# Performance work log

Hardware: AMD Instinct MI355X
Metric: run time of the kernel (lower is better)

The kernel has to match this reference:

```python
import jax, jax.numpy as jnp
import numpy as np

LEAK = 0.3          # config['leak_rate']
LAST_N = 8          # config['last_n_outputs']


def setup_inputs() -> dict:
    key = jax.random.key(0)
    k1, k2, k3, k4, k5 = jax.random.split(key, 5)
    B, T, F, H, O = 256, 1000, 64, 1024, 10
    x = jax.random.normal(k1, (B, T, F), dtype=jnp.float32)
    w_in = jax.random.normal(k2, (F, H), dtype=jnp.float32) * 0.2
    # reservoir matrix scaled to spectral radius ~0.9 (randn HxH has radius ~sqrt(H))
    w_r = jax.random.normal(k3, (H, H), dtype=jnp.float32) * (0.9 / np.sqrt(H))
    w_lin = jax.random.normal(k4, (O, H * LAST_N), dtype=jnp.float32) * 0.02
    b_lin = jax.random.normal(k5, (O,), dtype=jnp.float32) * 0.02
    return {"x": x, "w_in": w_in, "w_r": w_r, "w_lin": w_lin, "b_lin": b_lin}


def _esn_forward(x, w_in, w_r, w_lin, b_lin):
    B, T, F = x.shape
    H = w_in.shape[1]
    n = LAST_N
    # t = 0: h_0 = h_hat (no leaky combine per original code)
    h = jnp.tanh(x[:, 0, :] @ w_in)

    def step(h, xt):
        h_hat = jnp.tanh(xt @ w_in + h @ w_r)
        return (1.0 - LEAK) * h + LEAK * h_hat

    # steps 1 .. T-n-1: carry only, no outputs stored
    def body_nohist(h, xt):
        return step(h, xt), None

    xs_mid = jnp.swapaxes(x[:, 1:T - n, :], 0, 1)   # [T-n-1, B, F]
    h, _ = jax.lax.scan(body_nohist, h, xs_mid)

    # steps T-n .. T-1: keep states (out_list in original)
    def body_hist(h, xt):
        h = step(h, xt)
        return h, h

    xs_tail = jnp.swapaxes(x[:, T - n:, :], 0, 1)   # [n, B, F]
    _, hs = jax.lax.scan(body_hist, h, xs_tail)     # [n, B, H]

    # torch.cat(out_list, dim=1): oldest kept state first -> [B, n*H]
    feats = jnp.transpose(hs, (1, 0, 2)).reshape(B, n * H)
    return feats @ w_lin.T + b_lin


def reference(x, w_in, w_r, w_lin, b_lin):
    return _esn_forward(x, w_in, w_r, w_lin, b_lin)
```

## Files before the change

kernel.cpp:

```cpp
#include <hip/hip_runtime.h>
#include <math.h>

#define LEAK   0.3f
#define ONEML  0.7f

typedef unsigned short u16;
typedef unsigned int   u32;
typedef unsigned long long u64;
typedef __attribute__((ext_vector_type(4))) float f32x4;
typedef __attribute__((ext_vector_type(8))) short s16x8;

constexpr int B = 256, T = 1000, F = 64, H = 1024, O = 10, NTAIL = 8;
constexpr int TSTART  = T - NTAIL;
constexpr int KS      = 34;
constexpr int PSTRIDE = 1096;

constexpr size_t OFF_PACKED = 0;
constexpr size_t OFF_HGL    = 0x240000;
constexpr size_t OFF_FLAGS  = 0x340000;
constexpr size_t OFF_FEATS  = 0x344000;

__device__ __forceinline__ u16 f2bf(float f) {
  union { float f; u32 u; } v; v.f = f;
  u32 r = v.u + 0x7fffu + ((v.u >> 16) & 1u);
  return (u16)(r >> 16);
}

__device__ __forceinline__ float ftanh(float s) {
  const float sc = fminf(fmaxf(s, -9.0f), 9.0f);
  const float e2 = __builtin_amdgcn_exp2f(sc * 2.8853900817779268f);
  return 1.0f - 2.0f * __builtin_amdgcn_rcpf(e2 + 1.0f);
}

__global__ void esn_pack(const float* __restrict__ w_in, const float* __restrict__ w_r,
                         u16* __restrict__ packed) {
  int gid = blockIdx.x * 256 + threadIdx.x;
  if (gid >= 64 * KS * 64) return;
  int lane = gid & 63;
  int ks   = (gid >> 6) % KS;
  int nt   = gid / (KS * 64);
  int n    = nt * 16 + (lane & 15);
  int g    = lane >> 4;
  u16 v[8];
  #pragma unroll
  for (int jj = 0; jj < 8; ++jj) {
    int kk = 8 * g + jj;
    float w;
    if (ks < 2) w = w_in[(ks * 32 + kk) * H + n];
    else        w = w_r[((ks - 2) * 32 + kk) * H + n];
    v[jj] = f2bf(w);
  }
  u64* dst = (u64*)(packed + (size_t)gid * 8);
  dst[0] = ((const u64*)v)[0];
  dst[1] = ((const u64*)v)[1];
}

__global__ __launch_bounds__(256, 1) void esn_recur(const float* __restrict__ x,
    const u16* __restrict__ packed, u16* __restrict__ hgl,
    u32* __restrict__ flags, float* __restrict__ feats) {
  __shared__ u16 panel[2][16][PSTRIDE];
  __shared__ u16 forcepad[6144];

  const int tid  = threadIdx.x;
  const int lane = tid & 63, wv = tid >> 6;
  const int ci   = blockIdx.x >> 4;
  const int cj   = blockIdx.x & 15;
  const int g    = lane >> 4, m16 = lane & 15;
  const int nt   = cj * 4 + wv;
  const int cc   = nt * 16 + m16;
  const int bbase = ci * 16;
  const bool ownCols = ((tid >> 4) == cj);

  s16x8 bfrag[KS];
  #pragma unroll
  for (int ks = 0; ks < KS; ++ks)
    bfrag[ks] = *(const s16x8*)(packed + (((size_t)nt * KS + ks) * 64 + lane) * 8);

  float hreg[4] = {0.f, 0.f, 0.f, 0.f};

  for (int t = 0; t < T; ++t) {
    const int buf = t & 1;
    const int nb  = buf ^ 1;

    {
      const int r = tid >> 4;
      const int c = (tid & 15) * 4;
      const float4 v = *(const float4*)(x + (((size_t)(bbase + r)) * T + t) * (size_t)F + c);
      u16 o[4] = { f2bf(v.x), f2bf(v.y), f2bf(v.z), f2bf(v.w) };
      *(u64*)&panel[buf][r][c] = *(const u64*)o;
    }

    if (t > 0) {
      const u32 target = (u32)t;
      u32* fp = &flags[ci * 64 + lane];
      int guard = 0;
      for (;;) {
        u32 fv = __hip_atomic_load(fp, __ATOMIC_RELAXED, __HIP_MEMORY_SCOPE_AGENT);
        if (__all((int)(fv >= target))) break;
        if (++guard > (1 << 16)) break;
      }
      asm volatile("" ::: "memory");
    }

    if (t == 0) {
      #pragma unroll
      for (int it = 0; it < 16; ++it)
        *(u64*)&panel[buf][it][64 + tid * 4] = 0ULL;
    } else if (!ownCols) {
      const int pb = (t + 1) & 1;
      u64 vb[16];
      #pragma unroll
      for (int it = 0; it < 16; ++it)
        vb[it] = __hip_atomic_load(
            (const u64*)(hgl + ((((size_t)pb * 16 + ci) * 16 + it) * H + tid * 4)),
            __ATOMIC_RELAXED, __HIP_MEMORY_SCOPE_AGENT);
      #pragma unroll
      for (int it = 0; it < 16; ++it)
        *(u64*)&panel[buf][it][64 + tid * 4] = vb[it];
    }
    __syncthreads();

    f32x4 acc0 = {0.f,0.f,0.f,0.f}, acc1 = {0.f,0.f,0.f,0.f};
    #pragma unroll
    for (int ks = 0; ks < KS; ++ks) {
      s16x8 a = *(const s16x8*)&panel[buf][m16][ks * 32 + g * 8];
      if (ks & 1) acc1 = __builtin_amdgcn_mfma_f32_16x16x32_bf16(a, bfrag[ks], acc1, 0, 0, 0);
      else        acc0 = __builtin_amdgcn_mfma_f32_16x16x32_bf16(a, bfrag[ks], acc0, 0, 0, 0);
    }

    #pragma unroll
    for (int r = 0; r < 4; ++r) {
      const float s  = acc0[r] + acc1[r];
      const float th = ftanh(s);
      const float hn = (t == 0) ? th : (ONEML * hreg[r] + LEAK * th);
      hreg[r] = hn;
      const int rr = g * 4 + r;
      panel[nb][rr][64 + cc] = f2bf(hn);
      if (t >= TSTART)
        feats[((size_t)(bbase + rr)) * (H * NTAIL) + (t - TSTART) * H + cc] = hn;
    }

    asm volatile("s_waitcnt lgkmcnt(0)" ::: "memory");
    {
      const int r  = lane >> 2;
      const int c4 = (lane & 3) * 4;
      const u64 v = *(const u64*)&panel[nb][r][64 + nt * 16 + c4];
      __hip_atomic_store(
          (u64*)(hgl + ((((size_t)buf * 16 + ci) * 16 + r) * H + nt * 16 + c4)),
          v, __ATOMIC_RELAXED, __HIP_MEMORY_SCOPE_AGENT);
    }

    asm volatile("s_waitcnt vmcnt(0)" ::: "memory");
    if (lane == 0)
      __hip_atomic_store(&flags[ci * 64 + nt], (u32)(t + 1),
                         __ATOMIC_RELAXED, __HIP_MEMORY_SCOPE_AGENT);
  }
  if (tid == 255) ((volatile u16*)forcepad)[0] = (u16)lane;
}

__global__ __launch_bounds__(256) void esn_out(const float* __restrict__ feats,
    const float* __restrict__ w_lin, const float* __restrict__ b_lin,
    float* __restrict__ out) {
  const int b = blockIdx.x;
  const int tid = threadIdx.x;
  const int lane = tid & 63, wv = tid >> 6;
  float p[O];
  #pragma unroll
  for (int o = 0; o < O; ++o) p[o] = 0.f;
  const float* fr = feats + (size_t)b * (H * NTAIL);
  for (int idx = tid; idx < H * NTAIL; idx += 256) {
    const float f = fr[idx];
    #pragma unroll
    for (int o = 0; o < O; ++o) p[o] += f * w_lin[o * (H * NTAIL) + idx];
  }
  __shared__ float red[O][4];
  #pragma unroll
  for (int o = 0; o < O; ++o) {
    float v = p[o];
    for (int off = 32; off > 0; off >>= 1) v += __shfl_down(v, off);
    if (lane == 0) red[o][wv] = v;
  }
  __syncthreads();
  if (tid < O)
    out[b * O + tid] = red[tid][0] + red[tid][1] + red[tid][2] + red[tid][3] + b_lin[tid];
}

extern "C" void kernel_launch(void* const* d_in, const int* in_sizes, int n_in,
                              void* d_out, int out_size, void* d_ws, size_t ws_size,
                              hipStream_t stream) {
  const float* x     = (const float*)d_in[0];
  const float* w_in  = (const float*)d_in[1];
  const float* w_r   = (const float*)d_in[2];
  const float* w_lin = (const float*)d_in[3];
  const float* b_lin = (const float*)d_in[4];
  char* ws = (char*)d_ws;
  u16* packed = (u16*)(ws + OFF_PACKED);
  u16* hgl    = (u16*)(ws + OFF_HGL);
  u32* flags  = (u32*)(ws + OFF_FLAGS);
  float* feats= (float*)(ws + OFF_FEATS);
  float* out  = (float*)d_out;

  hipMemsetAsync(flags, 0, 4096 * sizeof(u32), stream);
  esn_pack<<<(64 * KS * 64 + 255) / 256, 256, 0, stream>>>(w_in, w_r, packed);

  void* args[] = { (void*)&x, (void*)&packed, (void*)&hgl, (void*)&flags, (void*)&feats };
  hipError_t rc = hipLaunchCooperativeKernel((void*)esn_recur, dim3(256), dim3(256),
                                             args, 0, stream);
  if (rc != hipSuccess)
    esn_recur<<<dim3(256), dim3(256), 0, stream>>>(x, packed, hgl, flags, feats);

  esn_out<<<B, 256, 0, stream>>>(feats, w_lin, b_lin, out);
}
```

Before: 3.270 ms.

## Replace store-drain before flag with per-column checksum validation of exchanged hidden state

Removes the vmcnt(0) wait that made each wave's hidden-state stores land before it published its step flag. Each column-tile now also writes a 17th row holding a per-column bf16 checksum XORed with the step number. Readers reload the 16 rows until the checksum matches, so a flag that becomes visible before its data is tolerated. Flags shrink to u16. This trades one full memory-fence stall per step for extra checksum arithmetic, an additional row load, and possible retry loops. Checksum collisions could silently let stale data through.

```diff
diff --git a/kernel.cpp b/kernel.cpp
--- a/kernel.cpp
+++ b/kernel.cpp
@@ -14,11 +14,13 @@
 constexpr int TSTART  = T - NTAIL;
 constexpr int KS      = 34;
 constexpr int PSTRIDE = 1096;
+constexpr int HROWS   = 17;
+
 
 constexpr size_t OFF_PACKED = 0;
 constexpr size_t OFF_HGL    = 0x240000;
-constexpr size_t OFF_FLAGS  = 0x340000;
-constexpr size_t OFF_FEATS  = 0x344000;
+constexpr size_t OFF_FLAGS  = 0x350000;
+constexpr size_t OFF_FEATS  = 0x354000;
 
 __device__ __forceinline__ u16 f2bf(float f) {
   union { float f; u32 u; } v; v.f = f;
@@ -57,7 +59,7 @@
 
 __global__ __launch_bounds__(256, 1) void esn_recur(const float* __restrict__ x,
     const u16* __restrict__ packed, u16* __restrict__ hgl,
-    u32* __restrict__ flags, float* __restrict__ feats) {
+    u16* __restrict__ flags, float* __restrict__ feats) {
   __shared__ u16 panel[2][16][PSTRIDE];
   __shared__ u16 forcepad[6144];
 
@@ -91,11 +93,11 @@
     }
 
     if (t > 0) {
-      const u32 target = (u32)t;
-      u32* fp = &flags[ci * 64 + lane];
+      const u16 target = (u16)t;
+      const u16* fp = flags + ci * 64 + lane;
       int guard = 0;
       for (;;) {
-        u32 fv = __hip_atomic_load(fp, __ATOMIC_RELAXED, __HIP_MEMORY_SCOPE_AGENT);
+        u16 fv = __hip_atomic_load(fp, __ATOMIC_RELAXED, __HIP_MEMORY_SCOPE_AGENT);
         if (__all((int)(fv >= target))) break;
         if (++guard > (1 << 16)) break;
       }
@@ -107,13 +109,37 @@
       for (int it = 0; it < 16; ++it)
         *(u64*)&panel[buf][it][64 + tid * 4] = 0ULL;
     } else if (!ownCols) {
+      const u32 stp = (u32)t & 0xffffu;
       const int pb = (t + 1) & 1;
-      u64 vb[16];
+      const u16* rbase = hgl + (((size_t)pb * 16 + ci) * HROWS) * H + tid * 4;
+      u64 vb[16], ck;
       #pragma unroll
       for (int it = 0; it < 16; ++it)
-        vb[it] = __hip_atomic_load(
-            (const u64*)(hgl + ((((size_t)pb * 16 + ci) * 16 + it) * H + tid * 4)),
-            __ATOMIC_RELAXED, __HIP_MEMORY_SCOPE_AGENT);
+        vb[it] = __hip_atomic_load((const u64*)(rbase + (size_t)it * H),
+                                   __ATOMIC_RELAXED, __HIP_MEMORY_SCOPE_AGENT);
+      ck = __hip_atomic_load((const u64*)(rbase + (size_t)16 * H),
+                             __ATOMIC_RELAXED, __HIP_MEMORY_SCOPE_AGENT);
+      int guard = 0;
+      for (;;) {
+        u32 bad = 0;
+        #pragma unroll
+        for (int c = 0; c < 4; ++c) {
+          u32 s = 0;
+          #pragma unroll
+          for (int it = 0; it < 16; ++it)
+            s += (u32)((vb[it] >> (16 * c)) & 0xffffu);
+          const u32 expect = (s & 0xffffu) ^ stp;
+          if (((u32)(ck >> (16 * c)) & 0xffffu) != expect) bad = 1;
+        }
+        if (!bad) break;
+        if (++guard > 4096) break;
+        #pragma unroll
+        for (int it = 0; it < 16; ++it)
+          vb[it] = __hip_atomic_load((const u64*)(rbase + (size_t)it * H),
+                                     __ATOMIC_RELAXED, __HIP_MEMORY_SCOPE_AGENT);
+        ck = __hip_atomic_load((const u64*)(rbase + (size_t)16 * H),
+                               __ATOMIC_RELAXED, __HIP_MEMORY_SCOPE_AGENT);
+      }
       #pragma unroll
       for (int it = 0; it < 16; ++it)
         *(u64*)&panel[buf][it][64 + tid * 4] = vb[it];
@@ -128,31 +154,39 @@
       else        acc0 = __builtin_amdgcn_mfma_f32_16x16x32_bf16(a, bfrag[ks], acc0, 0, 0, 0);
     }
 
+    u32 cs = 0;
     #pragma unroll
     for (int r = 0; r < 4; ++r) {
       const float s  = acc0[r] + acc1[r];
       const float th = ftanh(s);
       const float hn = (t == 0) ? th : (ONEML * hreg[r] + LEAK * th);
       hreg[r] = hn;
+      const u16 hb = f2bf(hn);
+      cs += (u32)hb;
       const int rr = g * 4 + r;
-      panel[nb][rr][64 + cc] = f2bf(hn);
+      panel[nb][rr][64 + cc] = hb;
       if (t >= TSTART)
         feats[((size_t)(bbase + rr)) * (H * NTAIL) + (t - TSTART) * H + cc] = hn;
     }
+    cs += (u32)__shfl_xor((int)cs, 16);
+    cs += (u32)__shfl_xor((int)cs, 32);
 
     asm volatile("s_waitcnt lgkmcnt(0)" ::: "memory");
     {
+      const size_t wb = (((size_t)buf * 16 + ci) * HROWS) * H;
       const int r  = lane >> 2;
       const int c4 = (lane & 3) * 4;
       const u64 v = *(const u64*)&panel[nb][r][64 + nt * 16 + c4];
-      __hip_atomic_store(
-          (u64*)(hgl + ((((size_t)buf * 16 + ci) * 16 + r) * H + nt * 16 + c4)),
-          v, __ATOMIC_RELAXED, __HIP_MEMORY_SCOPE_AGENT);
-    }
-
-    asm volatile("s_waitcnt vmcnt(0)" ::: "memory");
+      __hip_atomic_store((u64*)(hgl + wb + (size_t)r * H + nt * 16 + c4),
+                         v, __ATOMIC_RELAXED, __HIP_MEMORY_SCOPE_AGENT);
+      if (g == 0)
+        __hip_atomic_store(hgl + wb + (size_t)16 * H + cc,
+                           (u16)((cs & 0xffffu) ^ ((u32)(t + 1) & 0xffffu)),
+                           __ATOMIC_RELAXED, __HIP_MEMORY_SCOPE_AGENT);
+    }
+    asm volatile("" ::: "memory");
     if (lane == 0)
-      __hip_atomic_store(&flags[ci * 64 + nt], (u32)(t + 1),
+      __hip_atomic_store(&flags[ci * 64 + nt], (u16)(t + 1),
                          __ATOMIC_RELAXED, __HIP_MEMORY_SCOPE_AGENT);
   }
   if (tid == 255) ((volatile u16*)forcepad)[0] = (u16)lane;
@@ -196,11 +230,11 @@
   char* ws = (char*)d_ws;
   u16* packed = (u16*)(ws + OFF_PACKED);
   u16* hgl    = (u16*)(ws + OFF_HGL);
-  u32* flags  = (u32*)(ws + OFF_FLAGS);
+  u16* flags  = (u16*)(ws + OFF_FLAGS);
   float* feats= (float*)(ws + OFF_FEATS);
   float* out  = (float*)d_out;
 
-  hipMemsetAsync(flags, 0, 4096 * sizeof(u32), stream);
+  hipMemsetAsync(flags, 0, 4096, stream);
   esn_pack<<<(64 * KS * 64 + 255) / 256, 256, 0, stream>>>(w_in, w_r, packed);
 
   void* args[] = { (void*)&x, (void*)&packed, (void*)&hgl, (void*)&flags, (void*)&feats };
```

After: 3.589 ms. 9.8% more time.
